# Kernel tuning notes

Hardware: AMD Instinct MI355X
Metric: run time of the kernel (lower is better)

The kernel has to match this reference:

```python
import jax, jax.numpy as jnp
import numpy as np

B, L, HID = 2, 2048, 2048
H, KVH, HD = 8, 1, 256
GROUPS = H // KVH
THETA = 10000.0
NEG_INF = -1e9


def _rope_cos_sin(seq_len, hd):
    inv_freq = 1.0 / (THETA ** (jnp.arange(0, hd, 2, dtype=jnp.float32) / hd))
    t = jnp.arange(seq_len, dtype=jnp.float32)
    freqs = jnp.outer(t, inv_freq)                # [L, hd/2]
    emb = jnp.concatenate([freqs, freqs], axis=-1)  # [L, hd]
    return jnp.cos(emb), jnp.sin(emb)


def _rotate_half(x):
    x1, x2 = jnp.split(x, 2, axis=-1)
    return jnp.concatenate([-x2, x1], axis=-1)


def _apply_rope(x, cos, sin):
    # x: [B, h, L, hd]; cos/sin: [L, hd] broadcast over batch/heads
    return x * cos[None, None] + _rotate_half(x) * sin[None, None]


def setup_inputs() -> dict:
    key = jax.random.key(0)
    kx, kq, kk, kv, ko = jax.random.split(key, 5)
    s = lambda fan_in: 1.0 / np.sqrt(fan_in)
    x = jax.random.normal(kx, (B, L, HID), dtype=jnp.float32)
    Wq = jax.random.normal(kq, (HID, H * HD), dtype=jnp.float32) * s(HID)
    Wk = jax.random.normal(kk, (HID, KVH * HD), dtype=jnp.float32) * s(HID)
    Wv = jax.random.normal(kv, (HID, KVH * HD), dtype=jnp.float32) * s(HID)
    Wo = jax.random.normal(ko, (H * HD, HID), dtype=jnp.float32) * s(H * HD)
    # causal additive mask, same semantics as SDPA attn_mask (float, additive)
    causal = jnp.tril(jnp.ones((L, L), dtype=bool))
    mask = jnp.where(causal, 0.0, NEG_INF).astype(jnp.float32)[None, None]
    return {"x": x, "Wq": Wq, "Wk": Wk, "Wv": Wv, "Wo": Wo, "mask": mask}


def reference(x, Wq, Wk, Wv, Wo, mask):
    # projections -> [B, h, L, hd]
    q = (x @ Wq).reshape(B, L, H, HD).transpose(0, 2, 1, 3)
    k = (x @ Wk).reshape(B, L, KVH, HD).transpose(0, 2, 1, 3)
    v = (x @ Wv).reshape(B, L, KVH, HD).transpose(0, 2, 1, 3)
    cos, sin = _rope_cos_sin(L, HD)
    q = _apply_rope(q, cos, sin)
    k = _apply_rope(k, cos, sin)
    # GQA: replicate kv heads (repeat_interleave over head dim)
    k = jnp.repeat(k, GROUPS, axis=1)
    v = jnp.repeat(v, GROUPS, axis=1)
    scale = HD ** -0.5
    scores = jnp.einsum("bhqd,bhkd->bhqk", q, k) * scale + mask
    attn = jax.nn.softmax(scores.astype(jnp.float32), axis=-1).astype(q.dtype)
    out = jnp.einsum("bhqk,bhkd->bhqd", attn, v)
    out = out.transpose(0, 2, 1, 3).reshape(B, L, H * HD)
    return out @ Wo
```

## Files before the change

### kernel.cpp

```cpp
#include <hip/hip_runtime.h>

typedef unsigned short u16;
typedef __attribute__((ext_vector_type(8))) short short8x;
typedef __attribute__((ext_vector_type(4))) float f32x4;

#define B_ 2
#define L_ 2048
#define HID_ 2048
#define H_ 8
#define HD_ 256

__device__ __forceinline__ u16 f2bf(float f) {
  union { float f; unsigned u; } v; v.f = f;
  unsigned r = v.u + 0x7FFFu + ((v.u >> 16) & 1u);
  return (u16)(r >> 16);
}
__device__ __forceinline__ float bf2f(u16 u) {
  union { unsigned u; float f; } v; v.u = ((unsigned)u) << 16;
  return v.f;
}

__device__ __forceinline__ void gload_lds16(const void* g, void* l) {
  __builtin_amdgcn_global_load_lds((const __attribute__((address_space(1))) unsigned*)g,
                                   (__attribute__((address_space(3))) unsigned*)l, 16, 0, 0);
}

__global__ __launch_bounds__(256) void cvt_x_kernel(const float4* __restrict__ in,
                                                    u16* __restrict__ out) {
  int idx = blockIdx.x * 256 + threadIdx.x;
  float4 v = in[idx];
  u16* o = out + (size_t)idx * 4;
  o[0] = f2bf(v.x); o[1] = f2bf(v.y); o[2] = f2bf(v.z); o[3] = f2bf(v.w);
}

__global__ __launch_bounds__(256) void cvt_wt_kernel(const float* __restrict__ W,
                                                     u16* __restrict__ Wt, int K, int N) {
  __shared__ float tile[32][33];
  int n0 = blockIdx.x * 32, k0 = blockIdx.y * 32;
  int tx = threadIdx.x, ty = threadIdx.y;
#pragma unroll
  for (int i = 0; i < 32; i += 8)
    tile[ty + i][tx] = W[(size_t)(k0 + ty + i) * N + n0 + tx];
  __syncthreads();
#pragma unroll
  for (int i = 0; i < 32; i += 8)
    Wt[(size_t)(n0 + ty + i) * K + k0 + tx] = f2bf(tile[tx][ty + i]);
}

__global__ __launch_bounds__(256) void rope_kernel(const u16* __restrict__ in,
                                                   u16* __restrict__ out, int nh_shift,
                                                   int in_stride, int in_off, float scale) {
  int idx = blockIdx.x * 256 + threadIdx.x;
  int nh = 1 << nh_shift;
  int d = idx & 127;
  int t = idx >> 7;
  int h = t & (nh - 1);
  int row = t >> nh_shift;
  int l = row & (L_ - 1);
  int b = row >> 11;
  size_t ibase = (size_t)row * in_stride + in_off + h * 256 + d;
  float x1 = bf2f(in[ibase]);
  float x2 = bf2f(in[ibase + 128]);
  float f = exp2f(-(float)d * (13.287712379549449f / 128.0f));
  float ang = (float)l * f;
  float s, c;
  sincosf(ang, &s, &c);
  size_t obase = ((size_t)(b * nh + h) * L_ + l) * 256 + d;
  out[obase] = f2bf((x1 * c - x2 * s) * scale);
  out[obase + 128] = f2bf((x2 * c + x1 * s) * scale);
}

__global__ __launch_bounds__(256) void vt_kernel(const u16* __restrict__ qkvproj,
                                                 u16* __restrict__ vt) {
  __shared__ u16 tile[32][33];
  int l0 = blockIdx.x * 32, d0 = blockIdx.y * 32, b = blockIdx.z;
  int tx = threadIdx.x, ty = threadIdx.y;
#pragma unroll
  for (int i = 0; i < 32; i += 8)
    tile[ty + i][tx] = qkvproj[((size_t)b * 2048 + l0 + ty + i) * 2560 + 2304 + d0 + tx];
  __syncthreads();
#pragma unroll
  for (int i = 0; i < 32; i += 8)
    vt[((size_t)b * 256 + d0 + ty + i) * 2048 + l0 + tx] = tile[tx][ty + i];
}

template <int F32OUT>
__global__ __launch_bounds__(256) void gemm_bt_kernel(const u16* __restrict__ A,
                                                      const u16* __restrict__ Bt,
                                                      void* __restrict__ Cv,
                                                      int M, int N, int K) {
  __shared__ __attribute__((aligned(16))) u16 As[128 * 32];
  __shared__ __attribute__((aligned(16))) u16 Bs[128 * 32];
  const int tid = threadIdx.x;
  const int lane = tid & 63;
  const int w = tid >> 6;
  const int wr = w >> 1, wc = w & 1;
  const int nbx = gridDim.x;
  int flat = blockIdx.y * nbx + blockIdx.x;
  int nwg = nbx * gridDim.y;
  int q8 = nwg >> 3, r8 = nwg & 7;
  int xcd = flat & 7, idx8 = flat >> 3;
  int neu = (xcd < r8 ? xcd * (q8 + 1) : r8 * (q8 + 1) + (xcd - r8) * q8) + idx8;
  const int m0 = (neu / nbx) * 128, n0 = (neu % nbx) * 128;
  const int l15 = lane & 15, l4 = lane >> 4;
  f32x4 acc[4][4] = {};
  for (int kt = 0; kt < K; kt += 32) {
#pragma unroll
    for (int i = 0; i < 2; ++i) {
      int c = tid + i * 256;
      int row = c >> 2, cin = c & 3;
      gload_lds16(A + (size_t)(m0 + row) * K + kt + cin * 8,
                  (char*)As + (i * 256 + w * 64) * 16);
      gload_lds16(Bt + (size_t)(n0 + row) * K + kt + cin * 8,
                  (char*)Bs + (i * 256 + w * 64) * 16);
    }
    __syncthreads();
    short8x a[4], b[4];
#pragma unroll
    for (int m = 0; m < 4; ++m)
      a[m] = *(const short8x*)(&As[(wr * 64 + m * 16 + l15) * 32 + l4 * 8]);
#pragma unroll
    for (int n = 0; n < 4; ++n)
      b[n] = *(const short8x*)(&Bs[(wc * 64 + n * 16 + l15) * 32 + l4 * 8]);
#pragma unroll
    for (int m = 0; m < 4; ++m)
#pragma unroll
      for (int n = 0; n < 4; ++n)
        acc[m][n] = __builtin_amdgcn_mfma_f32_16x16x32_bf16(a[m], b[n], acc[m][n], 0, 0, 0);
    __syncthreads();
  }
#pragma unroll
  for (int m = 0; m < 4; ++m) {
#pragma unroll
    for (int n = 0; n < 4; ++n) {
      int gcol = n0 + wc * 64 + n * 16 + l15;
#pragma unroll
      for (int r = 0; r < 4; ++r) {
        int grow = m0 + wr * 64 + m * 16 + l4 * 4 + r;
        if (F32OUT)
          ((float*)Cv)[(size_t)grow * N + gcol] = acc[m][n][r];
        else
          ((u16*)Cv)[(size_t)grow * N + gcol] = f2bf(acc[m][n][r]);
      }
    }
  }
}

__global__ __launch_bounds__(512) void flash_kernel(const u16* __restrict__ qb,
                                                    const u16* __restrict__ kb,
                                                    const u16* __restrict__ vt,
                                                    u16* __restrict__ attn_o) {
  __shared__ __attribute__((aligned(16))) u16 Kbuf[2][64 * 256];
  __shared__ __attribute__((aligned(16))) u16 Vbuf[2][256 * 64];
  __shared__ __attribute__((aligned(16))) u16 Ps[8 * 16 * 64];
  const int x = blockIdx.x;
  const int p = x >> 4;
  const int bh = x & 15;
  const int b = bh >> 3;
  const int h = bh & 7;
  const int tid = threadIdx.x, lane = tid & 63, w = tid >> 6;
  const int l15 = lane & 15, l4 = lane >> 4;
  const int j = (w < 4) ? (31 - p) : p;
  const int q0 = j * 64 + (w & 3) * 16;
  const int nt = (31 - p) + 1;

  const u16* qrow = qb + ((size_t)(b * 8 + h) * L_ + q0 + l15) * 256;
  short8x qf[8];
#pragma unroll
  for (int kc = 0; kc < 8; ++kc)
    qf[kc] = *(const short8x*)(qrow + kc * 32 + l4 * 8);

  f32x4 o[16] = {};
  float mrow = -3e38f, srow = 0.f;

  const u16* kbase = kb + (size_t)b * (L_ * 256);
  const u16* vbase = vt + (size_t)b * (256 * L_);

#define STAGE(t, s)                                                            \
  {                                                                            \
    _Pragma("unroll") for (int i2 = 0; i2 < 4; ++i2) {                         \
      int c = i2 * 512 + tid;                                                  \
      int rk = c >> 5, cck = c & 31, jk = cck ^ (rk & 7);                      \
      gload_lds16(kbase + (size_t)((t) * 64 + rk) * 256 + jk * 8,              \
                  (char*)&Kbuf[s][0] + (i2 * 512 + w * 64) * 16);              \
      int rd = c >> 3, ccv = c & 7, jv = ccv ^ (rd & 7);                       \
      gload_lds16(vbase + (size_t)rd * L_ + (t) * 64 + jv * 8,                 \
                  (char*)&Vbuf[s][0] + (i2 * 512 + w * 64) * 16);              \
    }                                                                          \
  }

  STAGE(0, 0);
  asm volatile("s_waitcnt vmcnt(0)" ::: "memory");
  __syncthreads();

  for (int t = 0; t < nt; ++t) {
    if (t + 1 < nt) STAGE(t + 1, (t + 1) & 1);
    if (t <= j) {
      const char* Kb = (const char*)&Kbuf[t & 1][0];
      const char* Vb = (const char*)&Vbuf[t & 1][0];

      f32x4 sacc[4] = {};
      __builtin_amdgcn_s_setprio(1);
#pragma unroll
      for (int kc = 0; kc < 8; ++kc)
#pragma unroll
        for (int n = 0; n < 4; ++n) {
          int row = n * 16 + l15;
          short8x kf = *(const short8x*)(Kb +
              ((row * 512 + kc * 64 + l4 * 16) ^ ((row & 7) << 4)));
          sacc[n] = __builtin_amdgcn_mfma_f32_16x16x32_bf16(kf, qf[kc], sacc[n], 0, 0, 0);
        }
      __builtin_amdgcn_s_setprio(0);
      float pp[4][4];
      const bool dm = (t == j);
      const int qg = q0 + l15;
      float pm = -3e38f;
#pragma unroll
      for (int n = 0; n < 4; ++n)
#pragma unroll
        for (int r = 0; r < 4; ++r) {
          int kvg = t * 64 + n * 16 + l4 * 4 + r;
          float v = sacc[n][r];
          if (dm && (kvg > qg)) v = -1e30f;
          pp[n][r] = v;
          pm = fmaxf(pm, v);
        }
      pm = fmaxf(pm, __shfl_xor(pm, 16));
      pm = fmaxf(pm, __shfl_xor(pm, 32));
      const bool defer = __all(pm <= mrow + 8.f);
      float mn, alpha;
      if (defer) {
        mn = mrow;
      } else {
        mn = fmaxf(mrow, pm);
        alpha = __expf(mrow - mn);
        mrow = mn;
      }
      float rs = 0.f;
#pragma unroll
      for (int n = 0; n < 4; ++n)
#pragma unroll
        for (int r = 0; r < 4; ++r) {
          pp[n][r] = __expf(pp[n][r] - mn);
          rs += pp[n][r];
        }
      rs += __shfl_xor(rs, 16);
      rs += __shfl_xor(rs, 32);
      if (defer) {
        srow += rs;
      } else {
        srow = srow * alpha + rs;
        float av[4];
#pragma unroll
        for (int r = 0; r < 4; ++r)
          av[r] = __shfl(alpha, l4 * 4 + r, 16);
#pragma unroll
        for (int ff = 0; ff < 16; ++ff) {
          o[ff][0] *= av[0]; o[ff][1] *= av[1];
          o[ff][2] *= av[2]; o[ff][3] *= av[3];
        }
      }
#pragma unroll
      for (int n = 0; n < 4; ++n)
#pragma unroll
        for (int r = 0; r < 4; r += 2) {
          unsigned pk;
          asm("v_cvt_pk_bf16_f32 %0, %1, %2" : "=v"(pk) : "v"(pp[n][r]), "v"(pp[n][r + 1]));
          *(unsigned*)((char*)Ps + w * 2048 +
                       ((l15 * 128 + (n * 16 + l4 * 4 + r) * 2) ^ ((l15 & 7) << 4))) = pk;
        }
      asm volatile("s_waitcnt lgkmcnt(0)" ::: "memory");
      short8x paf[2];
#pragma unroll
      for (int kc2 = 0; kc2 < 2; ++kc2)
        paf[kc2] = *(const short8x*)((const char*)Ps + w * 2048 +
            ((l15 * 128 + kc2 * 64 + l4 * 16) ^ ((l15 & 7) << 4)));
      __builtin_amdgcn_s_setprio(1);
#pragma unroll
      for (int kc2 = 0; kc2 < 2; ++kc2)
#pragma unroll
        for (int ff = 0; ff < 16; ++ff) {
          int rd = ff * 16 + l15;
          short8x vf = *(const short8x*)(Vb +
              ((rd * 128 + kc2 * 64 + l4 * 16) ^ ((rd & 7) << 4)));
          o[ff] = __builtin_amdgcn_mfma_f32_16x16x32_bf16(paf[kc2], vf, o[ff], 0, 0, 0);
        }
      __builtin_amdgcn_s_setprio(0);
    }
    asm volatile("s_waitcnt vmcnt(0)" ::: "memory");
    __syncthreads();
  }
  float sv[4];
#pragma unroll
  for (int r = 0; r < 4; ++r)
    sv[r] = __shfl(srow, l4 * 4 + r, 16);
#pragma unroll
  for (int r = 0; r < 4; ++r) {
    float inv = 1.0f / sv[r];
    int grow = q0 + l4 * 4 + r;
    size_t base = ((size_t)b * L_ + grow) * (size_t)(H_ * HD_) + h * 256;
#pragma unroll
    for (int ff = 0; ff < 16; ++ff)
      attn_o[base + ff * 16 + l15] = f2bf(o[ff][r] * inv);
  }
#undef STAGE
}

extern "C" void kernel_launch(void* const* d_in, const int* in_sizes, int n_in,
                              void* d_out, int out_size, void* d_ws, size_t ws_size,
                              hipStream_t stream) {
  const float* x  = (const float*)d_in[0];
  const float* Wq = (const float*)d_in[1];
  const float* Wk = (const float*)d_in[2];
  const float* Wv = (const float*)d_in[3];
  const float* Wo = (const float*)d_in[4];
  float* out = (float*)d_out;
  char* ws = (char*)d_ws;
  size_t off = 0;
  auto alloc = [&](size_t bytes) {
    void* p = ws + off;
    off = (off + bytes + 255) & ~(size_t)255;
    return p;
  };
  u16* wqkv_t  = (u16*)alloc(2560ull * 2048 * 2);
  u16* wo_t    = (u16*)alloc(2048ull * 2048 * 2);
  u16* xbf     = (u16*)alloc(4096ull * 2048 * 2);
  u16* qkvproj = (u16*)alloc(4096ull * 2560 * 2);
  u16* kb      = (u16*)alloc(4096ull * 256 * 2);
  u16* vtb     = (u16*)alloc(4096ull * 256 * 2);
  u16* qbuf    = xbf;
  u16* attn_o  = qkvproj;

  cvt_x_kernel<<<8192, 256, 0, stream>>>((const float4*)x, xbf);
  cvt_wt_kernel<<<dim3(64, 64), dim3(32, 8), 0, stream>>>(Wq, wqkv_t, 2048, 2048);
  cvt_wt_kernel<<<dim3(8, 64),  dim3(32, 8), 0, stream>>>(Wk, wqkv_t + 2048ull * 2048, 2048, 256);
  cvt_wt_kernel<<<dim3(8, 64),  dim3(32, 8), 0, stream>>>(Wv, wqkv_t + 2304ull * 2048, 2048, 256);
  cvt_wt_kernel<<<dim3(64, 64), dim3(32, 8), 0, stream>>>(Wo, wo_t, 2048, 2048);

  gemm_bt_kernel<0><<<dim3(20, 32), 256, 0, stream>>>(xbf, wqkv_t, qkvproj, 4096, 2560, 2048);

  rope_kernel<<<16384, 256, 0, stream>>>(qkvproj, qbuf, 3, 2560, 0, 0.0625f);
  rope_kernel<<<2048, 256, 0, stream>>>(qkvproj, kb, 0, 2560, 2048, 1.0f);
  vt_kernel<<<dim3(64, 8, 2), dim3(32, 8), 0, stream>>>(qkvproj, vtb);

  flash_kernel<<<256, 512, 0, stream>>>(qbuf, kb, vtb, attn_o);

  gemm_bt_kernel<1><<<dim3(16, 32), 256, 0, stream>>>(attn_o, wo_t, out, 4096, 2048, 2048);
}
```

Baseline: 237.1 us.

## Replace 128x128 GEMM with double-buffered 256x256 swizzled-LDS MFMA kernel

Replaces the projection GEMM with a 256x256 tile kernel using 512 threads, K-step 64 and double-buffered LDS. Global-to-LDS loads for the next tile are interleaved with MFMA phases, using barriers and s_setprio. An XOR swizzle on LDS addresses avoids bank conflicts. The intent is more data reuse per block and overlap of loads with compute. The cost is a grid of only 128–160 blocks, which underfills the CUs, plus heavy register use.

```diff
diff --git a/kernel.cpp b/kernel.cpp
--- a/kernel.cpp
+++ b/kernel.cpp
@@ -85,65 +85,136 @@
 }
 
 template <int F32OUT>
-__global__ __launch_bounds__(256) void gemm_bt_kernel(const u16* __restrict__ A,
+__global__ __launch_bounds__(512) void gemm256_kernel(const u16* __restrict__ A,
                                                       const u16* __restrict__ Bt,
                                                       void* __restrict__ Cv,
                                                       int M, int N, int K) {
-  __shared__ __attribute__((aligned(16))) u16 As[128 * 32];
-  __shared__ __attribute__((aligned(16))) u16 Bs[128 * 32];
-  const int tid = threadIdx.x;
-  const int lane = tid & 63;
-  const int w = tid >> 6;
-  const int wr = w >> 1, wc = w & 1;
+  __shared__ __attribute__((aligned(16))) u16 As[2][256 * 64];
+  __shared__ __attribute__((aligned(16))) u16 Bs[2][256 * 64];
+  const int tid = threadIdx.x, lane = tid & 63, w = tid >> 6;
+  const int wr = w >> 2, wc = w & 3;
+  const int l15 = lane & 15, l4 = lane >> 4;
   const int nbx = gridDim.x;
   int flat = blockIdx.y * nbx + blockIdx.x;
   int nwg = nbx * gridDim.y;
   int q8 = nwg >> 3, r8 = nwg & 7;
   int xcd = flat & 7, idx8 = flat >> 3;
   int neu = (xcd < r8 ? xcd * (q8 + 1) : r8 * (q8 + 1) + (xcd - r8) * q8) + idx8;
-  const int m0 = (neu / nbx) * 128, n0 = (neu % nbx) * 128;
-  const int l15 = lane & 15, l4 = lane >> 4;
-  f32x4 acc[4][4] = {};
-  for (int kt = 0; kt < K; kt += 32) {
-#pragma unroll
-    for (int i = 0; i < 2; ++i) {
-      int c = tid + i * 256;
-      int row = c >> 2, cin = c & 3;
-      gload_lds16(A + (size_t)(m0 + row) * K + kt + cin * 8,
-                  (char*)As + (i * 256 + w * 64) * 16);
-      gload_lds16(Bt + (size_t)(n0 + row) * K + kt + cin * 8,
-                  (char*)Bs + (i * 256 + w * 64) * 16);
+  const int m0 = (neu / nbx) * 256, n0 = (neu % nbx) * 256;
+  const int NT = K >> 6;
+
+  f32x4 acc[8][4] = {};
+  short8x a[4][2], b[4][2];
+
+#define STAGE_A(t, s)                                                           \
+  {                                                                             \
+    _Pragma("unroll") for (int i = 0; i < 4; ++i) {                             \
+      int c = i * 512 + tid;                                                    \
+      int row = c >> 3, j = (c & 7) ^ (row & 7);                                \
+      gload_lds16(A + (size_t)(m0 + row) * K + (t) * 64 + j * 8,                \
+                  (char*)&As[s][0] + (i * 512 + w * 64) * 16);                  \
+    }                                                                           \
+  }
+#define STAGE_B(t, s)                                                           \
+  {                                                                             \
+    _Pragma("unroll") for (int i = 0; i < 4; ++i) {                             \
+      int c = i * 512 + tid;                                                    \
+      int row = c >> 3, j = (c & 7) ^ (row & 7);                                \
+      gload_lds16(Bt + (size_t)(n0 + row) * K + (t) * 64 + j * 8,               \
+                  (char*)&Bs[s][0] + (i * 512 + w * 64) * 16);                  \
+    }                                                                           \
+  }
+#define RD_A(s, mi, ks)                                                         \
+  (*(const short8x*)((const char*)&As[s][0] +                                   \
+      ((((wr * 128 + (mi) * 16 + l15) * 128 + ((ks) * 4 + l4) * 16)) ^          \
+       ((l15 & 7) << 4))))
+#define RD_B(s, ni, ks)                                                         \
+  (*(const short8x*)((const char*)&Bs[s][0] +                                   \
+      ((((wc * 64 + (ni) * 16 + l15) * 128 + ((ks) * 4 + l4) * 16)) ^           \
+       ((l15 & 7) << 4))))
+
+  STAGE_A(0, 0);
+  STAGE_B(0, 0);
+  asm volatile("s_waitcnt vmcnt(0)" ::: "memory");
+  __builtin_amdgcn_s_barrier();
+
+  for (int t = 0; t < NT; ++t) {
+    const int s = t & 1;
+    const bool ns = (t + 1 < NT);
+#pragma unroll
+    for (int mi = 0; mi < 4; ++mi) { a[mi][0] = RD_A(s, mi, 0); a[mi][1] = RD_A(s, mi, 1); }
+#pragma unroll
+    for (int ni = 0; ni < 2; ++ni) { b[ni][0] = RD_B(s, ni, 0); b[ni][1] = RD_B(s, ni, 1); }
+    if (ns) STAGE_A(t + 1, s ^ 1);
+    __builtin_amdgcn_s_barrier();
+    __builtin_amdgcn_s_setprio(1);
+#pragma unroll
+    for (int mi = 0; mi < 4; ++mi)
+#pragma unroll
+      for (int ni = 0; ni < 2; ++ni) {
+        acc[mi][ni] = __builtin_amdgcn_mfma_f32_16x16x32_bf16(a[mi][0], b[ni][0], acc[mi][ni], 0, 0, 0);
+        acc[mi][ni] = __builtin_amdgcn_mfma_f32_16x16x32_bf16(a[mi][1], b[ni][1], acc[mi][ni], 0, 0, 0);
+      }
+    __builtin_amdgcn_s_setprio(0);
+    __builtin_amdgcn_s_barrier();
+#pragma unroll
+    for (int ni = 2; ni < 4; ++ni) { b[ni][0] = RD_B(s, ni, 0); b[ni][1] = RD_B(s, ni, 1); }
+    if (ns) STAGE_B(t + 1, s ^ 1);
+    __builtin_amdgcn_s_barrier();
+    __builtin_amdgcn_s_setprio(1);
+#pragma unroll
+    for (int mi = 0; mi < 4; ++mi)
+#pragma unroll
+      for (int ni = 2; ni < 4; ++ni) {
+        acc[mi][ni] = __builtin_amdgcn_mfma_f32_16x16x32_bf16(a[mi][0], b[ni][0], acc[mi][ni], 0, 0, 0);
+        acc[mi][ni] = __builtin_amdgcn_mfma_f32_16x16x32_bf16(a[mi][1], b[ni][1], acc[mi][ni], 0, 0, 0);
+      }
+    __builtin_amdgcn_s_setprio(0);
+    __builtin_amdgcn_s_barrier();
+#pragma unroll
+    for (int mi = 0; mi < 4; ++mi) { a[mi][0] = RD_A(s, mi + 4, 0); a[mi][1] = RD_A(s, mi + 4, 1); }
+    __builtin_amdgcn_s_barrier();
+    __builtin_amdgcn_s_setprio(1);
+#pragma unroll
+    for (int mi = 0; mi < 4; ++mi)
+#pragma unroll
+      for (int ni = 2; ni < 4; ++ni) {
+        acc[mi + 4][ni] = __builtin_amdgcn_mfma_f32_16x16x32_bf16(a[mi][0], b[ni][0], acc[mi + 4][ni], 0, 0, 0);
+        acc[mi + 4][ni] = __builtin_amdgcn_mfma_f32_16x16x32_bf16(a[mi][1], b[ni][1], acc[mi + 4][ni], 0, 0, 0);
+      }
+    __builtin_amdgcn_s_setprio(0);
+    __builtin_amdgcn_s_barrier();
+    __builtin_amdgcn_s_setprio(1);
+#pragma unroll
+    for (int mi = 0; mi < 4; ++mi)
+#pragma unroll
+      for (int ni = 0; ni < 2; ++ni) {
+        acc[mi + 4][ni] = __builtin_amdgcn_mfma_f32_16x16x32_bf16(a[mi][0], b[ni][0], acc[mi + 4][ni], 0, 0, 0);
+        acc[mi + 4][ni] = __builtin_amdgcn_mfma_f32_16x16x32_bf16(a[mi][1], b[ni][1], acc[mi + 4][ni], 0, 0, 0);
+      }
+    __builtin_amdgcn_s_setprio(0);
+    if (ns) asm volatile("s_waitcnt vmcnt(0)" ::: "memory");
+    __builtin_amdgcn_s_barrier();
+  }
+#pragma unroll
+  for (int mi = 0; mi < 8; ++mi) {
+#pragma unroll
+    for (int ni = 0; ni < 4; ++ni) {
+      int gcol = n0 + wc * 64 + ni * 16 + l15;
+#pragma unroll
+      for (int r = 0; r < 4; ++r) {
+        int grow = m0 + wr * 128 + mi * 16 + l4 * 4 + r;
+        if (F32OUT)
+          ((float*)Cv)[(size_t)grow * N + gcol] = acc[mi][ni][r];
+        else
+          ((u16*)Cv)[(size_t)grow * N + gcol] = f2bf(acc[mi][ni][r]);
+      }
     }
-    __syncthreads();
-    short8x a[4], b[4];
-#pragma unroll
-    for (int m = 0; m < 4; ++m)
-      a[m] = *(const short8x*)(&As[(wr * 64 + m * 16 + l15) * 32 + l4 * 8]);
-#pragma unroll
-    for (int n = 0; n < 4; ++n)
-      b[n] = *(const short8x*)(&Bs[(wc * 64 + n * 16 + l15) * 32 + l4 * 8]);
-#pragma unroll
-    for (int m = 0; m < 4; ++m)
-#pragma unroll
-      for (int n = 0; n < 4; ++n)
-        acc[m][n] = __builtin_amdgcn_mfma_f32_16x16x32_bf16(a[m], b[n], acc[m][n], 0, 0, 0);
-    __syncthreads();
-  }
-#pragma unroll
-  for (int m = 0; m < 4; ++m) {
-#pragma unroll
-    for (int n = 0; n < 4; ++n) {
-      int gcol = n0 + wc * 64 + n * 16 + l15;
-#pragma unroll
-      for (int r = 0; r < 4; ++r) {
-        int grow = m0 + wr * 64 + m * 16 + l4 * 4 + r;
-        if (F32OUT)
-          ((float*)Cv)[(size_t)grow * N + gcol] = acc[m][n][r];
-        else
-          ((u16*)Cv)[(size_t)grow * N + gcol] = f2bf(acc[m][n][r]);
-      }
-    }
-  }
+  }
+#undef STAGE_A
+#undef STAGE_B
+#undef RD_A
+#undef RD_B
 }
 
 __global__ __launch_bounds__(512) void flash_kernel(const u16* __restrict__ qb,
@@ -337,7 +408,7 @@
   cvt_wt_kernel<<<dim3(8, 64),  dim3(32, 8), 0, stream>>>(Wv, wqkv_t + 2304ull * 2048, 2048, 256);
   cvt_wt_kernel<<<dim3(64, 64), dim3(32, 8), 0, stream>>>(Wo, wo_t, 2048, 2048);
 
-  gemm_bt_kernel<0><<<dim3(20, 32), 256, 0, stream>>>(xbf, wqkv_t, qkvproj, 4096, 2560, 2048);
+  gemm256_kernel<0><<<dim3(10, 16), 512, 0, stream>>>(xbf, wqkv_t, qkvproj, 4096, 2560, 2048);
 
   rope_kernel<<<16384, 256, 0, stream>>>(qkvproj, qbuf, 3, 2560, 0, 0.0625f);
   rope_kernel<<<2048, 256, 0, stream>>>(qkvproj, kb, 0, 2560, 2048, 1.0f);
@@ -345,5 +416,5 @@
 
   flash_kernel<<<256, 512, 0, stream>>>(qbuf, kb, vtb, attn_o);
 
-  gemm_bt_kernel<1><<<dim3(16, 32), 256, 0, stream>>>(attn_o, wo_t, out, 4096, 2048, 2048);
-}
+  gemm256_kernel<1><<<dim3(8, 16), 512, 0, stream>>>(attn_o, wo_t, out, 4096, 2048, 2048);
+}
```

Measured after the change: 242.0 us. 1.02x slower.
